# Optimization experiments

Hardware: AMD Instinct MI355X
Metric: run time of the kernel (lower is better)

## Reference

```python
import jax, jax.numpy as jnp
import numpy as np

IN_CH, OUT_CH, K, UP = 512, 256, 3, 2
WSCALE = float(1.0 / np.sqrt(K * K * IN_CH))  # use_wscale gain / sqrt(fan_in), lr_mul=1
ACT_GAIN = float(np.sqrt(2.0))                # lrelu def_gain
CLAMP = 256.0                                  # conv_clamp * runtime_gain(=1)
FIR_PAD = 1                                    # px0+pxt = px1+pxt = 1 (derived in forward)

def _fir_filter():
    # upfirdn2d.setup_filter([1,3,3,1]): outer product then normalize to sum 1
    f1 = jnp.array([1.0, 3.0, 3.0, 1.0], jnp.float32)
    f2 = jnp.outer(f1, f1)
    return f2 / jnp.sum(f2)  # (4,4), sums to 1

def setup_inputs() -> dict:
    key = jax.random.key(0)
    k1, k2 = jax.random.split(key)
    return {
        "x": jax.random.normal(k1, (16, IN_CH, 64, 64), jnp.float32),
        "weight": jax.random.normal(k2, (OUT_CH, IN_CH, K, K), jnp.float32),
        "bias": jnp.zeros((OUT_CH,), jnp.float32),
    }

def _forward(x, weight, bias):
    w = weight * WSCALE  # runtime weight scaling
    # torch conv_transpose2d(x, w.transpose(0,1), stride=UP, padding=0)
    # == lhs-dilated correlation with spatially flipped kernel, pad K-1 each side
    k = w[:, :, ::-1, ::-1]
    y = jax.lax.conv_general_dilated(
        x, k, window_strides=(1, 1),
        padding=((K - 1, K - 1), (K - 1, K - 1)),
        lhs_dilation=(UP, UP),
        dimension_numbers=('NCHW', 'OIHW', 'NCHW'))  # (N, OUT_CH, 129, 129)
    # upfirdn2d(up=1, padding=(1,1,1,1), gain=UP**2):
    # pad, then depthwise conv with flipped filter scaled by gain**(ndim/2)=UP*UP
    f = _fir_filter() * (UP * UP)
    y = jnp.pad(y, ((0, 0), (0, 0), (FIR_PAD, FIR_PAD), (FIR_PAD, FIR_PAD)))
    fk = jnp.broadcast_to(f[::-1, ::-1][None, None], (OUT_CH, 1, 4, 4))
    y = jax.lax.conv_general_dilated(
        y, fk, (1, 1), 'VALID',
        feature_group_count=OUT_CH,
        dimension_numbers=('NCHW', 'OIHW', 'NCHW'))  # (N, OUT_CH, 128, 128)
    # bias_act: bias add, leaky_relu(0.2), gain sqrt(2), clamp +-256
    y = y + bias[None, :, None, None]
    y = jnp.where(y >= 0, y, 0.2 * y) * ACT_GAIN
    return jnp.clip(y, -CLAMP, CLAMP)

def reference(x, weight, bias):
    return _forward(x, weight, bias)
```

## Files before the change

kernel.cpp:

```cpp
#include <hip/hip_runtime.h>
#include <hip/hip_bf16.h>

#define NIMG 16
#define IN_CH 512
#define OUT_CH 256
#define HIN 64
#define HOUT 128
#define HP 66

#define WSCALE 0.014731391f
#define ACT_GAIN 1.41421356237f
#define CLAMP_V 256.0f

typedef __attribute__((ext_vector_type(8))) short bf16x8;
typedef __attribute__((ext_vector_type(4))) float f32x4;
typedef __attribute__((ext_vector_type(16))) float f32x16;

__device__ __constant__ float c_G[2][3][3] = {
    {{0.00f, 0.25f, 0.75f}, {0.75f, 0.75f, 0.25f}, {0.25f, 0.00f, 0.00f}},
    {{0.00f, 0.00f, 0.25f}, {0.25f, 0.75f, 0.75f}, {0.75f, 0.25f, 0.00f}}
};

#define XBF_BYTES ((size_t)NIMG * 64 * HP * HP * 16)
#define EBF_BYTES ((size_t)9 * 64 * 1024 * 16)
#define WS_NEED (XBF_BYTES + EBF_BYTES)

__global__ __launch_bounds__(256) void xpose_kernel(const float* __restrict__ x,
                                                    __hip_bfloat16* __restrict__ xbf) {
    const int n = blockIdx.z;
    const int hp = blockIdx.y;
    const int c0 = blockIdx.x << 6;
    const int tid = threadIdx.x;
    const int sgb = c0 >> 3;
    const bf16x8 zero = {0, 0, 0, 0, 0, 0, 0, 0};

    if (hp == 0 || hp == HP - 1) {
        for (int idx = tid; idx < 8 * HP; idx += 256) {
            int s3 = idx / HP, wp = idx - s3 * HP;
            size_t a = (((size_t)(n * 64 + sgb + s3) * HP + hp) * HP + wp);
            *(bf16x8*)((char*)xbf + a * 16) = zero;
        }
        return;
    }
    __shared__ float tile[64][65];
    {
        int cc = tid >> 6, w = tid & 63;
        for (int cb = 0; cb < 64; cb += 4)
            tile[cb + cc][w] =
                x[(((size_t)n * IN_CH + c0 + cb + cc) * HIN + (hp - 1)) * HIN + w];
    }
    __syncthreads();
    {
        int s3 = tid >> 5, wq = tid & 31;
#pragma unroll
        for (int wb = 0; wb < 64; wb += 32) {
            int wimg = wb + wq;
            bf16x8 v;
#pragma unroll
            for (int k = 0; k < 8; ++k) {
                __hip_bfloat16 b = __float2bfloat16(tile[s3 * 8 + k][wimg]);
                v[k] = *reinterpret_cast<short*>(&b);
            }
            size_t a = (((size_t)(n * 64 + sgb + s3) * HP + hp) * HP + (wimg + 1));
            *(bf16x8*)((char*)xbf + a * 16) = v;
        }
        if (tid < 16) {
            int s3h = tid >> 1, wph = (tid & 1) ? (HP - 1) : 0;
            size_t a = (((size_t)(n * 64 + sgb + s3h) * HP + hp) * HP + wph);
            *(bf16x8*)((char*)xbf + a * 16) = zero;
        }
    }
}

__global__ __launch_bounds__(256) void build_ebf_kernel(const float* __restrict__ w,
                                                        __hip_bfloat16* __restrict__ ebf) {
    int gid = blockIdx.x * 256 + threadIdx.x;
    if (gid >= OUT_CH * IN_CH) return;
    int oc = gid >> 9, c = gid & 511;
    int sg = c >> 3, ce = c & 7;
    float wm[3][3];
    const float* wp = w + (size_t)gid * 9;
#pragma unroll
    for (int a = 0; a < 3; ++a)
#pragma unroll
        for (int b = 0; b < 3; ++b) wm[a][b] = wp[a * 3 + b] * WSCALE;
#pragma unroll
    for (int i = 0; i < 3; ++i)
#pragma unroll
        for (int j = 0; j < 3; ++j)
#pragma unroll
            for (int pu = 0; pu < 2; ++pu)
#pragma unroll
                for (int pv = 0; pv < 2; ++pv) {
                    float s = 0.f;
#pragma unroll
                    for (int a = 0; a < 3; ++a)
#pragma unroll
                        for (int b = 0; b < 3; ++b)
                            s += wm[a][b] * c_G[pu][i][a] * c_G[pv][j][b];
                    int row = oc * 4 + pu * 2 + pv;
                    ebf[(((size_t)(i * 3 + j) * 64 + sg) * 1024 + row) * 8 + ce] =
                        __float2bfloat16(s);
                }
}

#define MFMA4(AF, BF)                                                                       \
    do {                                                                                    \
        acc[0] = __builtin_amdgcn_mfma_f32_32x32x16_bf16((AF)[0], (BF)[0], acc[0], 0, 0, 0);\
        acc[1] = __builtin_amdgcn_mfma_f32_32x32x16_bf16((AF)[0], (BF)[1], acc[1], 0, 0, 0);\
        acc[2] = __builtin_amdgcn_mfma_f32_32x32x16_bf16((AF)[1], (BF)[0], acc[2], 0, 0, 0);\
        acc[3] = __builtin_amdgcn_mfma_f32_32x32x16_bf16((AF)[1], (BF)[1], acc[3], 0, 0, 0);\
    } while (0)

#define ASTEP 557568
#define AJ_FJ (-3902960)
#define AJ_FI (-3901952)
#define BSTEP 131072

#define GLL(SRC, DSTOFF)                                                          \
    __builtin_amdgcn_global_load_lds(                                             \
        (const __attribute__((address_space(1))) unsigned int*)(SRC),             \
        (__attribute__((address_space(3))) unsigned int*)(ldsW + (DSTOFF)), 16, 0, 0)

#define TILE_ITER(PAR, TT, SP, LAST)                                              \
    {                                                                             \
        const int PB = (PAR) << 16;                                               \
        const int NPB = ((PAR) ^ 1) << 16;                                        \
            \
        if (SP) {                                                                 \
            GLL(xbc + sA0 + voffA, NPB);                                          \
            GLL(xbc + sA1 + voffA, NPB + 16384);                                  \
            GLL(ebc + sB0 + voffB, NPB + 32768);                                  \
            GLL(ebc + sB1 + voffB, NPB + 49152);                                  \
        }                                                                         \
        sA0 += (((TT) & 7) == 6) ? (((TT) == 22 || (TT) == 46) ? AJ_FI : AJ_FJ)   \
                                 : ASTEP;                                         \
        sA1 += (((TT) & 7) == 6) ? (((TT) == 22 || (TT) == 46) ? AJ_FI : AJ_FJ)   \
                                 : ASTEP;                                         \
        sB0 += BSTEP;                                                             \
        sB1 += BSTEP;                                                             \
                                                  \
        aE[0] = *(const bf16x8*)&lds[A0 + PB];                                    \
        aE[1] = *(const bf16x8*)&lds[A1 + PB];                                    \
        bE[0] = *(const bf16x8*)&lds[B0 + PB];                                    \
        bE[1] = *(const bf16x8*)&lds[B1 + PB];                                    \
        aO[0] = *(const bf16x8*)&lds[A0 + PB + 8192];                             \
        aO[1] = *(const bf16x8*)&lds[A1 + PB + 8192];                             \
        bO[0] = *(const bf16x8*)&lds[B0 + PB + 8192];                             \
        bO[1] = *(const bf16x8*)&lds[B1 + PB + 8192];                             \
        asm volatile("s_waitcnt lgkmcnt(4)" ::: "memory");                        \
        __builtin_amdgcn_sched_barrier(0);                                        \
        __builtin_amdgcn_s_setprio(1);                                            \
        MFMA4(aE, bE);                                                            \
        __builtin_amdgcn_s_setprio(0);                                            \
                                                                \
        aE[0] = *(const bf16x8*)&lds[A0 + PB + 16384];                            \
        aE[1] = *(const bf16x8*)&lds[A1 + PB + 16384];                            \
        bE[0] = *(const bf16x8*)&lds[B0 + PB + 16384];                            \
        bE[1] = *(const bf16x8*)&lds[B1 + PB + 16384];                            \
        asm volatile("s_waitcnt lgkmcnt(4)" ::: "memory");                        \
        __builtin_amdgcn_sched_barrier(0);                                        \
        __builtin_amdgcn_s_setprio(1);                                            \
        MFMA4(aO, bO);                                                            \
        __builtin_amdgcn_s_setprio(0);                                            \
                                                                \
        aO[0] = *(const bf16x8*)&lds[A0 + PB + 24576];                            \
        aO[1] = *(const bf16x8*)&lds[A1 + PB + 24576];                            \
        bO[0] = *(const bf16x8*)&lds[B0 + PB + 24576];                            \
        bO[1] = *(const bf16x8*)&lds[B1 + PB + 24576];                            \
        asm volatile("s_waitcnt lgkmcnt(4)" ::: "memory");                        \
        __builtin_amdgcn_sched_barrier(0);                                        \
        __builtin_amdgcn_s_setprio(1);                                            \
        MFMA4(aE, bE);                                                            \
        __builtin_amdgcn_s_setprio(0);                                            \
        asm volatile("s_waitcnt lgkmcnt(0)" ::: "memory");                        \
        __builtin_amdgcn_sched_barrier(0);                                        \
        __builtin_amdgcn_s_setprio(1);                                            \
        MFMA4(aO, bO);                                                            \
        __builtin_amdgcn_s_setprio(0);                                            \
        if (!(LAST)) {                                                            \
            asm volatile("s_waitcnt vmcnt(0)" ::: "memory");                      \
            __builtin_amdgcn_s_barrier();                                         \
            __builtin_amdgcn_sched_barrier(0);                                    \
        }                                                                         \
    }

__global__ __launch_bounds__(1024) void mfma_conv8_kernel(
    const __hip_bfloat16* __restrict__ xbf, const __hip_bfloat16* __restrict__ ebf,
    const float* __restrict__ bias, float* __restrict__ out) {
    __shared__ __align__(16) char lds[131072];

    const int tid = threadIdx.x;
    const int lane = tid & 63;
    const int wid = tid >> 6;
    const int wy = wid >> 2;
    const int wx = wid & 3;

    const int bid = blockIdx.x;
    const int wkid = ((bid & 7) << 7) + (bid >> 3);
    const int mtile = wkid >> 2;
    const int ntile = wkid & 3;
    const int n = mtile >> 4;
    const int sub = mtile & 15;
    const int qh0 = (sub >> 2) << 4;
    const int qw0 = (sub & 3) << 4;
    const int n0 = ntile << 8;

    const int slice = wid & 3;
    const int rb = wid >> 2;

    f32x16 acc[4];
#pragma unroll
    for (int j = 0; j < 4; ++j) acc[j] = (f32x16)(0.f);

    char* ldsW = lds + (slice << 12) + (rb << 10);
    const char* xbc = (const char*)xbf;
    const char* ebc = (const char*)ebf;

    const int q = lane ^ ((lane & 32) ? 4 : 0) ^ ((slice & 1) ? 4 : 0);
    const int voffA =
        ((((n << 6) + slice) * HP + qh0 + (rb << 2) + (q >> 4)) * HP + qw0 +
         (q & 15)) * 16;
    const int voffB = (slice << 14) + ((n0 + (rb << 6) + q) << 4);

    const int sl = lane >> 5;
    const int l31 = lane & 31;
    const int sx = sl ? 64 : 0;
    const int A0 = (sl << 12) + (wy << 10) + ((l31 << 4) ^ sx);
    const int A1 = (sl << 12) + (wy << 10) + 512 + ((l31 << 4) ^ 64 ^ sx);
    const int B0 = 32768 + (sl << 12) + (wx << 10) + ((l31 << 4) ^ sx);
    const int B1 = 32768 + (sl << 12) + (wx << 10) + 512 + ((l31 << 4) ^ 64 ^ sx);

    int sA0 = 8 * 69696;
    int sA1 = 12 * 69696;
    int sB0 = 8 * 16384;
    int sB1 = 12 * 16384;

    GLL(xbc + voffA, 0);
    GLL(xbc + voffA + 4 * 69696, 16384);
    GLL(ebc + voffB, 32768);
    GLL(ebc + voffB + 4 * 16384, 49152);
    asm volatile("s_waitcnt vmcnt(0)" ::: "memory");
    __builtin_amdgcn_s_barrier();
    __builtin_amdgcn_sched_barrier(0);

    bf16x8 aE[2], aO[2], bE[2], bO[2];

#pragma unroll 1
    for (int tt = 0; tt < 70; tt += 2) {
        TILE_ITER(0, tt, 1, 0);
        TILE_ITER(1, tt + 1, 1, 0);
    }
    TILE_ITER(0, 70, 1, 0);
    TILE_ITER(1, 71, 0, 1);

    float bv[2];
#pragma unroll
    for (int nt = 0; nt < 2; ++nt)
        bv[nt] = bias[(n0 + (wx << 6) + (nt << 5) + l31) >> 2];
#pragma unroll
    for (int j = 0; j < 4; ++j) {
        const int mt = j >> 1, nt = j & 1;
        const int nn = n0 + (wx << 6) + (nt << 5) + l31;
        const int oc = nn >> 2, pu = (nn >> 1) & 1, pv = nn & 1;
#pragma unroll
        for (int v = 0; v < 16; ++v) {
            const int m = (wy << 6) + (mt << 5) + (v & 3) + ((v >> 2) << 3) + (sl << 2);
            const int qr = m >> 4, qc = m & 15;
            const int hb = 2 * (qh0 + qr), wb = 2 * (qw0 + qc);
            float val = acc[j][v] + bv[nt];
            val = (val >= 0.f ? val : 0.2f * val) * ACT_GAIN;
            val = fminf(fmaxf(val, -CLAMP_V), CLAMP_V);
            out[(((size_t)n * OUT_CH + oc) * HOUT + (hb + pu)) * HOUT + (wb + pv)] = val;
        }
    }
}

__global__ void build_e_kernel(const float* __restrict__ w, float* __restrict__ e_ws) {
    int gid = blockIdx.x * blockDim.x + threadIdx.x;
    if (gid >= OUT_CH * IN_CH) return;
    float wm[3][3];
    const float* wp = w + (size_t)gid * 9;
#pragma unroll
    for (int a = 0; a < 3; ++a)
#pragma unroll
        for (int b = 0; b < 3; ++b) wm[a][b] = wp[a * 3 + b] * WSCALE;
    float* op = e_ws + (size_t)gid * 36;
#pragma unroll
    for (int i = 0; i < 3; ++i)
#pragma unroll
        for (int j = 0; j < 3; ++j)
#pragma unroll
            for (int pu = 0; pu < 2; ++pu)
#pragma unroll
                for (int pv = 0; pv < 2; ++pv) {
                    float s = 0.f;
#pragma unroll
                    for (int a = 0; a < 3; ++a)
#pragma unroll
                        for (int b = 0; b < 3; ++b)
                            s += wm[a][b] * c_G[pu][i][a] * c_G[pv][j][b];
                    op[(i * 3 + j) * 4 + pu * 2 + pv] = s;
                }
}

#define OGB 8
#define CB 8
#define QT 16
__global__ __launch_bounds__(256) void fused_conv_kernel(
    const float* __restrict__ x, const float* __restrict__ e_ws,
    const float* __restrict__ bias, float* __restrict__ out) {
    __shared__ float sX[CB][18][19];
    __shared__ float4 sE[OGB * CB * 9];
    const int tid = threadIdx.x;
    const int o2 = tid >> 7;
    const int qy = (tid >> 3) & 15;
    const int qxp = tid & 7;
    const int tileIdx = blockIdx.x;
    const int hq0 = (tileIdx >> 2) * QT;
    const int wq0 = (tileIdx & 3) * QT;
    const int o0 = blockIdx.y * OGB;
    const int n = blockIdx.z;
    float4 acc[2][4];
#pragma unroll
    for (int q = 0; q < 2; ++q)
#pragma unroll
        for (int oo = 0; oo < 4; ++oo) acc[q][oo] = make_float4(0.f, 0.f, 0.f, 0.f);
    for (int c0 = 0; c0 < IN_CH; c0 += CB) {
        for (int idx = tid; idx < CB * 18 * 18; idx += 256) {
            int cc = idx / 324;
            int rem = idx - cc * 324;
            int r = rem / 18;
            int col = rem - r * 18;
            int h = hq0 - 1 + r;
            int ww = wq0 - 1 + col;
            float v = 0.f;
            if (h >= 0 && h < HIN && ww >= 0 && ww < HIN)
                v = x[(((size_t)n * IN_CH + (c0 + cc)) * HIN + h) * HIN + ww];
            sX[cc][r][col] = v;
        }
        {
            float* sEf = (float*)sE;
            for (int idx = tid; idx < OGB * CB * 36; idx += 256) {
                int ol = idx / (CB * 36);
                int rem = idx - ol * (CB * 36);
                sEf[ol * (CB * 36) + rem] =
                    e_ws[((size_t)(o0 + ol) * IN_CH + c0) * 36 + rem];
            }
        }
        __syncthreads();
#pragma unroll 1
        for (int cc = 0; cc < CB; ++cc) {
#pragma unroll
            for (int i = 0; i < 3; ++i) {
#pragma unroll
                for (int j = 0; j < 3; ++j) {
                    float xv0 = sX[cc][qy + i][2 * qxp + j];
                    float xv1 = sX[cc][qy + i][2 * qxp + 1 + j];
#pragma unroll
                    for (int oo = 0; oo < 4; ++oo) {
                        float4 e = sE[((o2 * 4 + oo) * CB + cc) * 9 + i * 3 + j];
                        acc[0][oo].x += xv0 * e.x; acc[0][oo].y += xv0 * e.y;
                        acc[0][oo].z += xv0 * e.z; acc[0][oo].w += xv0 * e.w;
                        acc[1][oo].x += xv1 * e.x; acc[1][oo].y += xv1 * e.y;
                        acc[1][oo].z += xv1 * e.z; acc[1][oo].w += xv1 * e.w;
                    }
                }
            }
        }
        __syncthreads();
    }
#pragma unroll
    for (int q = 0; q < 2; ++q) {
        int qx = 2 * qxp + q;
        int u0 = 2 * (hq0 + qy);
        int v0 = 2 * (wq0 + qx);
#pragma unroll
        for (int oo = 0; oo < 4; ++oo) {
            int o = o0 + o2 * 4 + oo;
            float b = bias[o];
            float vals[4] = {acc[q][oo].x, acc[q][oo].y, acc[q][oo].z, acc[q][oo].w};
#pragma unroll
            for (int p = 0; p < 4; ++p) {
                int pu = p >> 1, pv = p & 1;
                float v = vals[p] + b;
                v = (v >= 0.f ? v : 0.2f * v) * ACT_GAIN;
                v = fminf(fmaxf(v, -CLAMP_V), CLAMP_V);
                out[(((size_t)n * OUT_CH + o) * HOUT + (u0 + pu)) * HOUT + (v0 + pv)] = v;
            }
        }
    }
}

extern "C" void kernel_launch(void* const* d_in, const int* in_sizes, int n_in,
                              void* d_out, int out_size, void* d_ws, size_t ws_size,
                              hipStream_t stream) {
    const float* x = (const float*)d_in[0];
    const float* w = (const float*)d_in[1];
    const float* bias = (const float*)d_in[2];
    float* out = (float*)d_out;

    if (ws_size >= WS_NEED) {
        __hip_bfloat16* xbf = (__hip_bfloat16*)d_ws;
        __hip_bfloat16* ebf = (__hip_bfloat16*)((char*)d_ws + XBF_BYTES);
        xpose_kernel<<<dim3(8, HP, NIMG), 256, 0, stream>>>(x, xbf);
        build_ebf_kernel<<<(OUT_CH * IN_CH + 255) / 256, 256, 0, stream>>>(w, ebf);
        mfma_conv8_kernel<<<dim3(1024), 1024, 0, stream>>>(xbf, ebf, bias, out);
    } else {
        float* e_ws = (float*)d_ws;
        build_e_kernel<<<(OUT_CH * IN_CH + 255) / 256, 256, 0, stream>>>(w, e_ws);
        dim3 grid(16, OUT_CH / OGB, NIMG);
        fused_conv_kernel<<<grid, 256, 0, stream>>>(x, e_ws, bias, out);
    }
}
```

Baseline: 679.0 us.

## Load weight fragments directly from global into registers, halve LDS staging

The B (weight) operand is no longer staged through LDS. Each wave now loads its MFMA B fragments straight from global memory into registers, with a shifted layout offset. LDS then holds only the A tiles, which halves the shared allocation, and the A global-to-LDS copies are split across the iteration with a barrier after each half. This removes the LDS write/read traffic for weights and frees LDS, at the cost of global-load latency on the MFMA critical path. It relies on vmcnt waits and extra barriers to keep the pipeline correct.

```diff
diff --git a/kernel.cpp b/kernel.cpp
--- a/kernel.cpp
+++ b/kernel.cpp
@@ -122,73 +122,71 @@
         (const __attribute__((address_space(1))) unsigned int*)(SRC),             \
         (__attribute__((address_space(3))) unsigned int*)(ldsW + (DSTOFF)), 16, 0, 0)
 
-#define TILE_ITER(PAR, TT, SP, LAST)                                              \
+#define TILE_ITER(PAR, TT, SP, VMW, LGK3, LAST)                                   \
     {                                                                             \
-        const int PB = (PAR) << 16;                                               \
-        const int NPB = ((PAR) ^ 1) << 16;                                        \
-            \
-        if (SP) {                                                                 \
-            GLL(xbc + sA0 + voffA, NPB);                                          \
-            GLL(xbc + sA1 + voffA, NPB + 16384);                                  \
-            GLL(ebc + sB0 + voffB, NPB + 32768);                                  \
-            GLL(ebc + sB1 + voffB, NPB + 49152);                                  \
-        }                                                                         \
+        const int PB = (PAR) << 15;                                               \
+        const int NPB = ((PAR) ^ 1) << 15;                                        \
+           \
+        bO[0] = *(const bf16x8*)(ebc + sB + voffB2 + 32768);                      \
+        bO[1] = *(const bf16x8*)(ebc + sB + voffB2 + 32768 + 512);                \
+        if (SP) GLL(xbc + sA0 + voffA, NPB);                                      \
         sA0 += (((TT) & 7) == 6) ? (((TT) == 22 || (TT) == 46) ? AJ_FI : AJ_FJ)   \
                                  : ASTEP;                                         \
-        sA1 += (((TT) & 7) == 6) ? (((TT) == 22 || (TT) == 46) ? AJ_FI : AJ_FJ)   \
-                                 : ASTEP;                                         \
-        sB0 += BSTEP;                                                             \
-        sB1 += BSTEP;                                                             \
-                                                  \
-        aE[0] = *(const bf16x8*)&lds[A0 + PB];                                    \
-        aE[1] = *(const bf16x8*)&lds[A1 + PB];                                    \
-        bE[0] = *(const bf16x8*)&lds[B0 + PB];                                    \
-        bE[1] = *(const bf16x8*)&lds[B1 + PB];                                    \
         aO[0] = *(const bf16x8*)&lds[A0 + PB + 8192];                             \
         aO[1] = *(const bf16x8*)&lds[A1 + PB + 8192];                             \
-        bO[0] = *(const bf16x8*)&lds[B0 + PB + 8192];                             \
-        bO[1] = *(const bf16x8*)&lds[B1 + PB + 8192];                             \
-        asm volatile("s_waitcnt lgkmcnt(4)" ::: "memory");                        \
+        asm volatile("s_waitcnt " VMW ::: "memory");                              \
+        asm volatile("s_waitcnt lgkmcnt(2)" ::: "memory");                        \
         __builtin_amdgcn_sched_barrier(0);                                        \
         __builtin_amdgcn_s_setprio(1);                                            \
         MFMA4(aE, bE);                                                            \
         __builtin_amdgcn_s_setprio(0);                                            \
-                                                                \
+        __builtin_amdgcn_s_barrier();                                             \
+        __builtin_amdgcn_sched_barrier(0);                                        \
+                      \
+        bE[0] = *(const bf16x8*)(ebc + sB + voffB2 + 65536);                      \
+        bE[1] = *(const bf16x8*)(ebc + sB + voffB2 + 65536 + 512);                \
         aE[0] = *(const bf16x8*)&lds[A0 + PB + 16384];                            \
         aE[1] = *(const bf16x8*)&lds[A1 + PB + 16384];                            \
-        bE[0] = *(const bf16x8*)&lds[B0 + PB + 16384];                            \
-        bE[1] = *(const bf16x8*)&lds[B1 + PB + 16384];                            \
-        asm volatile("s_waitcnt lgkmcnt(4)" ::: "memory");                        \
+        asm volatile("s_waitcnt lgkmcnt(2)" ::: "memory");                        \
         __builtin_amdgcn_sched_barrier(0);                                        \
         __builtin_amdgcn_s_setprio(1);                                            \
         MFMA4(aO, bO);                                                            \
         __builtin_amdgcn_s_setprio(0);                                            \
-                                                                \
+           \
+        bO[0] = *(const bf16x8*)(ebc + sB + voffB2 + 98304);                      \
+        bO[1] = *(const bf16x8*)(ebc + sB + voffB2 + 98304 + 512);                \
+        if (SP) GLL(xbc + sA1 + voffA, NPB + 16384);                              \
+        sA1 += (((TT) & 7) == 6) ? (((TT) == 22 || (TT) == 46) ? AJ_FI : AJ_FJ)   \
+                                 : ASTEP;                                         \
+        sB += BSTEP;                                                              \
         aO[0] = *(const bf16x8*)&lds[A0 + PB + 24576];                            \
         aO[1] = *(const bf16x8*)&lds[A1 + PB + 24576];                            \
-        bO[0] = *(const bf16x8*)&lds[B0 + PB + 24576];                            \
-        bO[1] = *(const bf16x8*)&lds[B1 + PB + 24576];                            \
-        asm volatile("s_waitcnt lgkmcnt(4)" ::: "memory");                        \
+        asm volatile("s_waitcnt " VMW ::: "memory");                              \
+        asm volatile("s_waitcnt lgkmcnt(2)" ::: "memory");                        \
         __builtin_amdgcn_sched_barrier(0);                                        \
         __builtin_amdgcn_s_setprio(1);                                            \
         MFMA4(aE, bE);                                                            \
         __builtin_amdgcn_s_setprio(0);                                            \
-        asm volatile("s_waitcnt lgkmcnt(0)" ::: "memory");                        \
+        __builtin_amdgcn_s_barrier();                                             \
+        __builtin_amdgcn_sched_barrier(0);                                        \
+           \
+        if (!(LAST)) {                                                            \
+            bE[0] = *(const bf16x8*)(ebc + sB + voffB2);                          \
+            bE[1] = *(const bf16x8*)(ebc + sB + voffB2 + 512);                    \
+            aE[0] = *(const bf16x8*)&lds[A0 + NPB];                               \
+            aE[1] = *(const bf16x8*)&lds[A1 + NPB];                               \
+        }                                                                         \
+        asm volatile("s_waitcnt " LGK3 ::: "memory");                             \
         __builtin_amdgcn_sched_barrier(0);                                        \
         __builtin_amdgcn_s_setprio(1);                                            \
         MFMA4(aO, bO);                                                            \
         __builtin_amdgcn_s_setprio(0);                                            \
-        if (!(LAST)) {                                                            \
-            asm volatile("s_waitcnt vmcnt(0)" ::: "memory");                      \
-            __builtin_amdgcn_s_barrier();                                         \
-            __builtin_amdgcn_sched_barrier(0);                                    \
-        }                                                                         \
     }
 
 __global__ __launch_bounds__(1024) void mfma_conv8_kernel(
     const __hip_bfloat16* __restrict__ xbf, const __hip_bfloat16* __restrict__ ebf,
     const float* __restrict__ bias, float* __restrict__ out) {
-    __shared__ __align__(16) char lds[131072];
+    __shared__ __align__(16) char lds[65536];
 
     const int tid = threadIdx.x;
     const int lane = tid & 63;
@@ -221,38 +219,37 @@
     const int voffA =
         ((((n << 6) + slice) * HP + qh0 + (rb << 2) + (q >> 4)) * HP + qw0 +
          (q & 15)) * 16;
-    const int voffB = (slice << 14) + ((n0 + (rb << 6) + q) << 4);
-
     const int sl = lane >> 5;
     const int l31 = lane & 31;
+    const int voffB2 = (sl << 14) + ((n0 + (wx << 6) + l31) << 4);
+
     const int sx = sl ? 64 : 0;
     const int A0 = (sl << 12) + (wy << 10) + ((l31 << 4) ^ sx);
     const int A1 = (sl << 12) + (wy << 10) + 512 + ((l31 << 4) ^ 64 ^ sx);
-    const int B0 = 32768 + (sl << 12) + (wx << 10) + ((l31 << 4) ^ sx);
-    const int B1 = 32768 + (sl << 12) + (wx << 10) + 512 + ((l31 << 4) ^ 64 ^ sx);
 
     int sA0 = 8 * 69696;
     int sA1 = 12 * 69696;
-    int sB0 = 8 * 16384;
-    int sB1 = 12 * 16384;
+    int sB = 0;
+
+    bf16x8 aE[2], aO[2], bE[2], bO[2];
 
     GLL(xbc + voffA, 0);
     GLL(xbc + voffA + 4 * 69696, 16384);
-    GLL(ebc + voffB, 32768);
-    GLL(ebc + voffB + 4 * 16384, 49152);
+    bE[0] = *(const bf16x8*)(ebc + voffB2);
+    bE[1] = *(const bf16x8*)(ebc + voffB2 + 512);
     asm volatile("s_waitcnt vmcnt(0)" ::: "memory");
     __builtin_amdgcn_s_barrier();
     __builtin_amdgcn_sched_barrier(0);
-
-    bf16x8 aE[2], aO[2], bE[2], bO[2];
+    aE[0] = *(const bf16x8*)&lds[A0];
+    aE[1] = *(const bf16x8*)&lds[A1];
 
 #pragma unroll 1
     for (int tt = 0; tt < 70; tt += 2) {
-        TILE_ITER(0, tt, 1, 0);
-        TILE_ITER(1, tt + 1, 1, 0);
-    }
-    TILE_ITER(0, 70, 1, 0);
-    TILE_ITER(1, 71, 0, 1);
+        TILE_ITER(0, tt, 1, "vmcnt(5)", "lgkmcnt(2)", 0);
+        TILE_ITER(1, tt + 1, 1, "vmcnt(5)", "lgkmcnt(2)", 0);
+    }
+    TILE_ITER(0, 70, 1, "vmcnt(5)", "lgkmcnt(2)", 0);
+    TILE_ITER(1, 71, 0, "vmcnt(0)", "lgkmcnt(0)", 1);
 
     float bv[2];
 #pragma unroll
```

After: 738.1 us. +8.7%, slower.
